# Optimization experiments

Hardware: AMD Instinct MI355X
Metric: run time of the kernel (lower is better)

The kernel has to match this reference:

```python
import jax, jax.numpy as jnp
import numpy as np

N_NODES = 20000
N_EDGES = 320000
N_GRAPHS = 16
NEG_SLOPE = 0.2


def gat_layer(x, src, dst, W, al, ar, b):
    # x: [N, F_in]; W: [F_in, H*D]; al/ar: [H, D]; b: [H*D]
    H, D = al.shape
    N = x.shape[0]
    f = (x @ W).reshape(N, H, D)                      # projected features [N,H,D]
    el = jnp.sum(f * al[None], axis=-1)                # [N,H]
    er = jnp.sum(f * ar[None], axis=-1)                # [N,H]
    e = jax.nn.leaky_relu(el[src] + er[dst], NEG_SLOPE)  # [E,H]
    # numerically stable segment softmax over incoming edges of each dst node
    m = jax.ops.segment_max(e, dst, num_segments=N)    # [N,H]
    m = jnp.where(jnp.isfinite(m), m, 0.0)
    ex = jnp.exp(e - m[dst])                           # [E,H]
    denom = jax.ops.segment_sum(ex, dst, num_segments=N)  # [N,H]
    msg = ex[:, :, None] * f[src]                      # [E,H,D]
    num = jax.ops.segment_sum(msg, dst, num_segments=N)   # [N,H,D]
    rst = num / jnp.where(denom > 0, denom, 1.0)[:, :, None]
    return rst + b.reshape(1, H, D)


def setup_inputs() -> dict:
    key = jax.random.key(0)
    ks = jax.random.split(key, 16)
    in_dim, hid, H = 128, 128, 3
    x = jax.random.normal(ks[0], (N_NODES, in_dim), dtype=jnp.float32)
    src = jax.random.randint(ks[1], (N_EDGES,), 0, N_NODES, dtype=jnp.int32)
    dst = jax.random.randint(ks[2], (N_EDGES,), 0, N_NODES, dtype=jnp.int32)
    graph_ids = jnp.sort(jax.random.randint(ks[3], (N_NODES,), 0, N_GRAPHS, dtype=jnp.int32))
    s = lambda d: 1.0 / np.sqrt(d)
    W1 = jax.random.normal(ks[4], (in_dim, H * hid), jnp.float32) * s(in_dim)
    al1 = jax.random.normal(ks[5], (H, hid), jnp.float32) * s(hid)
    ar1 = jax.random.normal(ks[6], (H, hid), jnp.float32) * s(hid)
    b1 = jnp.zeros((H * hid,), jnp.float32)
    W2 = jax.random.normal(ks[7], (H * hid, hid), jnp.float32) * s(H * hid)
    al2 = jax.random.normal(ks[8], (1, hid), jnp.float32) * s(hid)
    ar2 = jax.random.normal(ks[9], (1, hid), jnp.float32) * s(hid)
    b2 = jnp.zeros((hid,), jnp.float32)
    linW = jax.random.normal(ks[10], (hid, hid), jnp.float32) * s(hid)
    linb = jnp.zeros((hid,), jnp.float32)
    return dict(x=x, src=src, dst=dst, graph_ids=graph_ids, W1=W1, al1=al1,
                ar1=ar1, b1=b1, W2=W2, al2=al2, ar2=ar2, b2=b2, linW=linW, linb=linb)


def reference(x, src, dst, graph_ids, W1, al1, ar1, b1, W2, al2, ar2, b2, linW, linb):
    h = gat_layer(x, src, dst, W1, al1, ar1, b1)       # [N,3,hid]
    h = jax.nn.elu(h.reshape(h.shape[0], -1))          # [N,3*hid]
    h = gat_layer(h, src, dst, W2, al2, ar2, b2)       # [N,1,hid]
    h = h.squeeze(1)                                   # [N,hid]
    # dgl.mean_nodes over batched graph
    sums = jax.ops.segment_sum(h, graph_ids, num_segments=N_GRAPHS)      # [G,hid]
    cnts = jax.ops.segment_sum(jnp.ones_like(graph_ids, jnp.float32), graph_ids, num_segments=N_GRAPHS)
    hg = sums / jnp.maximum(cnts, 1.0)[:, None]
    return jax.nn.relu(hg @ linW + linb)
```

## Files before the change

### kernel.cpp

```cpp
#include <hip/hip_runtime.h>
#include <hip/hip_bf16.h>

#define NN 20000
#define NE 320000
#define NG 16
#define PSPLIT 32
#define NSCANB 79


__global__ void hist_kernel(const int* __restrict__ dst, int* __restrict__ indeg, int E) {
  int e = blockIdx.x * 256 + threadIdx.x;
  if (e < E) atomicAdd(&indeg[dst[e]], 1);
}

__global__ void scan1_kernel(const int* __restrict__ in, int* __restrict__ outp,
                             int* __restrict__ bsum, int n) {
  int b = blockIdx.x, t = threadIdx.x;
  int i = b * 256 + t;
  int lane = t & 63, wv = t >> 6;
  __shared__ int ws[4];
  int v = (i < n) ? in[i] : 0;
  int x = v;
#pragma unroll
  for (int off = 1; off < 64; off <<= 1) {
    int y = __shfl_up(x, off);
    if (lane >= off) x += y;
  }
  if (lane == 63) ws[wv] = x;
  __syncthreads();
  int add = 0;
  for (int w2 = 0; w2 < wv; w2++) add += ws[w2];
  x += add;
  if (i < n) outp[i] = x - v;
  if (t == 255) bsum[b] = x;
}

__global__ void scan2_kernel(const int* __restrict__ bsum, int* __restrict__ boff,
                             int* __restrict__ rp_end, int nb) {
  int t = threadIdx.x;
  int lane = t & 63, wv = t >> 6;
  __shared__ int ws[2];
  int v = (t < nb) ? bsum[t] : 0;
  int x = v;
#pragma unroll
  for (int off = 1; off < 64; off <<= 1) {
    int y = __shfl_up(x, off);
    if (lane >= off) x += y;
  }
  if (lane == 63) ws[wv] = x;
  __syncthreads();
  if (wv == 1) x += ws[0];
  if (t < nb) boff[t] = x - v;
  if (t == 127) *rp_end = x;
}

__global__ void scan3_kernel(int* __restrict__ outp, const int* __restrict__ boff, int n) {
  int i = blockIdx.x * 256 + threadIdx.x;
  if (i < n) outp[i] += boff[blockIdx.x];
}

__global__ void scatter_kernel(const int* __restrict__ src, const int* __restrict__ dst,
                               const int* __restrict__ rowptr, int* __restrict__ cursor,
                               int* __restrict__ csr_src, int E) {
  int e = blockIdx.x * 256 + threadIdx.x;
  if (e < E) {
    int d = dst[e];
    int p = atomicAdd(&cursor[d], 1);
    csr_src[rowptr[d] + p] = src[e];
  }
}


__global__ void prep_wlr_kernel(const float* __restrict__ W1, const float* __restrict__ al1,
                                const float* __restrict__ ar1, float* __restrict__ wlr) {
  int t = blockIdx.x * 256 + threadIdx.x;
  if (t >= 768) return;
  int k = t & 127;
  int j = t >> 7;
  int h = j % 3;
  const float* av = (j < 3 ? al1 : ar1) + h * 128;
  const float* wrow = W1 + (size_t)k * 384 + h * 128;
  float s = 0.f;
#pragma unroll 4
  for (int d = 0; d < 128; d++) s += wrow[d] * av[d];
  wlr[j * 128 + k] = s;
}

__global__ void elr_kernel(const float* __restrict__ x, const float* __restrict__ wlr,
                           float* __restrict__ el, float* __restrict__ er, int N) {
  __shared__ float wl_s[768];
  int t = threadIdx.x;
  for (int i = t; i < 768; i += 256) wl_s[i] = wlr[i];
  __syncthreads();
  int w = (blockIdx.x * 256 + t) >> 6;
  int lane = t & 63;
  if (w >= N) return;
  float v0 = x[(size_t)w * 128 + lane], v1 = x[(size_t)w * 128 + 64 + lane];
  float s[6];
#pragma unroll
  for (int j = 0; j < 6; j++) s[j] = v0 * wl_s[j * 128 + lane] + v1 * wl_s[j * 128 + 64 + lane];
#pragma unroll
  for (int off = 32; off; off >>= 1)
#pragma unroll
    for (int j = 0; j < 6; j++) s[j] += __shfl_down(s[j], off);
  if (lane == 0) {
    el[w * 3 + 0] = s[0]; el[w * 3 + 1] = s[1]; el[w * 3 + 2] = s[2];
    er[w * 3 + 0] = s[3]; er[w * 3 + 1] = s[4]; er[w * 3 + 2] = s[5];
  }
}


__global__ void aggregate_x_kernel(const float* __restrict__ x, const float* __restrict__ el,
                                   const float* __restrict__ er, const int* __restrict__ rowptr,
                                   const int* __restrict__ csr_src, float* __restrict__ aggx) {
  int n = blockIdx.x;
  int t = threadIdx.x;
  __shared__ float wbuf[3][128];
  __shared__ int sbuf[128];
  __shared__ float red[6];
  __shared__ float4 accbuf[3][4][32];
  int rs = rowptr[n];
  int deg = rowptr[n + 1] - rs;
  float er0 = er[n * 3 + 0], er1 = er[n * 3 + 1], er2 = er[n * 3 + 2];
  float p0 = 0.f, p1 = 0.f, p2 = 0.f;
  int g = t >> 5, dq = t & 31;
  const float* xd = x + dq * 4;
  float4 a0 = make_float4(0, 0, 0, 0), a1 = a0, a2 = a0;
  for (int base = 0; base < deg; base += 128) {
    int cnt = min(128, deg - base);
    if (t < cnt) {
      int s = csr_src[rs + base + t];
      sbuf[t] = s;
      float e0 = el[s * 3 + 0] + er0, e1 = el[s * 3 + 1] + er1, e2 = el[s * 3 + 2] + er2;
      e0 = e0 > 0.f ? e0 : 0.2f * e0;
      e1 = e1 > 0.f ? e1 : 0.2f * e1;
      e2 = e2 > 0.f ? e2 : 0.2f * e2;
      float w0 = __expf(e0), w1 = __expf(e1), w2 = __expf(e2);
      wbuf[0][t] = w0; wbuf[1][t] = w1; wbuf[2][t] = w2;
      p0 += w0; p1 += w1; p2 += w2;
    }
    __syncthreads();
    int j = g;
    for (; j + 4 < cnt; j += 8) {
      int s0 = sbuf[j], s1 = sbuf[j + 4];
      float4 v0 = *(const float4*)(xd + (size_t)s0 * 128);
      float4 v1 = *(const float4*)(xd + (size_t)s1 * 128);
      float w00 = wbuf[0][j], w01 = wbuf[1][j], w02 = wbuf[2][j];
      float w10 = wbuf[0][j + 4], w11 = wbuf[1][j + 4], w12 = wbuf[2][j + 4];
      a0.x += w00 * v0.x + w10 * v1.x; a0.y += w00 * v0.y + w10 * v1.y;
      a0.z += w00 * v0.z + w10 * v1.z; a0.w += w00 * v0.w + w10 * v1.w;
      a1.x += w01 * v0.x + w11 * v1.x; a1.y += w01 * v0.y + w11 * v1.y;
      a1.z += w01 * v0.z + w11 * v1.z; a1.w += w01 * v0.w + w11 * v1.w;
      a2.x += w02 * v0.x + w12 * v1.x; a2.y += w02 * v0.y + w12 * v1.y;
      a2.z += w02 * v0.z + w12 * v1.z; a2.w += w02 * v0.w + w12 * v1.w;
    }
    for (; j < cnt; j += 4) {
      int s = sbuf[j];
      float4 v = *(const float4*)(xd + (size_t)s * 128);
      float w0 = wbuf[0][j], w1 = wbuf[1][j], w2 = wbuf[2][j];
      a0.x += w0 * v.x; a0.y += w0 * v.y; a0.z += w0 * v.z; a0.w += w0 * v.w;
      a1.x += w1 * v.x; a1.y += w1 * v.y; a1.z += w1 * v.z; a1.w += w1 * v.w;
      a2.x += w2 * v.x; a2.y += w2 * v.y; a2.z += w2 * v.z; a2.w += w2 * v.w;
    }
    __syncthreads();
  }
  for (int off = 32; off; off >>= 1) {
    p0 += __shfl_down(p0, off);
    p1 += __shfl_down(p1, off);
    p2 += __shfl_down(p2, off);
  }
  int wv = t >> 6, ln = t & 63;
  if (ln == 0) { red[wv * 3 + 0] = p0; red[wv * 3 + 1] = p1; red[wv * 3 + 2] = p2; }
  accbuf[0][g][dq] = a0;
  accbuf[1][g][dq] = a1;
  accbuf[2][g][dq] = a2;
  __syncthreads();
  if (t < 96) {
    int h = t >> 5, d = t & 31;
    float4 s0 = accbuf[h][0][d], s1 = accbuf[h][1][d], s2 = accbuf[h][2][d], s3 = accbuf[h][3][d];
    float dn = red[h] + red[3 + h];
    float inv = dn > 0.f ? 1.f / dn : 0.f;
    float4 r;
    r.x = (s0.x + s1.x + s2.x + s3.x) * inv;
    r.y = (s0.y + s1.y + s2.y + s3.y) * inv;
    r.z = (s0.z + s1.z + s2.z + s3.z) * inv;
    r.w = (s0.w + s1.w + s2.w + s3.w) * inv;
    *(float4*)&aggx[(size_t)n * 384 + h * 128 + d * 4] = r;
  }
}


template <int NCB, bool SPLIT, bool BIAS_ELU>
__launch_bounds__(256, 2)
__global__ void gemm_8x8_kernel(const float* __restrict__ A, int lda,
                                const float* __restrict__ B, int ldb,
                                float* __restrict__ C, int ldc,
                                const float* __restrict__ bias) {
  __shared__ float4 As4[128 * 9];
  __shared__ float4 Bs4[32 * 33];
  int t = threadIdx.x;
  int tm = t >> 4, tn = t & 15;

  constexpr int NROWT = 157;
  constexpr int NWG = NROWT * NCB;
  constexpr int QW = NWG >> 3, RW = NWG & 7;
  int o = blockIdx.x;
  int xcd = o & 7, i8 = o >> 3;
  int wgid = (xcd < RW ? xcd * (QW + 1) : RW * (QW + 1) + (xcd - RW) * QW) + i8;
  int rt = wgid / NCB, cb = wgid - rt * NCB;
  int m0 = rt * 128;

  const float* Ab = A + (size_t)(cb * 128);
  const float* Bb = SPLIT ? B + (size_t)(cb * 128) * ldb : B + cb * 128;
  float* Cb = SPLIT ? C + (size_t)cb * NN * ldc : C + cb * 128;

  const float* sA[4];
  int dA[4];
#pragma unroll
  for (int p = 0; p < 4; ++p) {
    int r = p * 32 + (t >> 3);
    int row = m0 + r;
    if (row >= NN) row = NN - 1;
    sA[p] = Ab + (size_t)row * lda + (t & 7) * 4;
    dA[p] = r * 9 + (t & 7);
  }
  const float* sB[4];
  int dB[4];
#pragma unroll
  for (int p = 0; p < 4; ++p) {
    int kk = p * 8 + (t >> 5);
    sB[p] = Bb + (size_t)kk * ldb + (t & 31) * 4;
    dB[p] = kk * 33 + (t & 31);
  }

  float acc[8][8];
#pragma unroll
  for (int i = 0; i < 8; ++i)
#pragma unroll
    for (int c = 0; c < 8; ++c) acc[i][c] = 0.f;

  float4 pa[4], pb[4];
#pragma unroll
  for (int p = 0; p < 4; ++p) {
    pa[p] = *(const float4*)sA[p];
    pb[p] = *(const float4*)sB[p];
  }

  constexpr int NT = 4;
  for (int tk = 0; tk < NT; ++tk) {
#pragma unroll
    for (int p = 0; p < 4; ++p) {
      As4[dA[p]] = pa[p];
      Bs4[dB[p]] = pb[p];
    }
    __syncthreads();
    if (tk + 1 < NT) {
      int ko = (tk + 1) * 32;
#pragma unroll
      for (int p = 0; p < 4; ++p) {
        pa[p] = *(const float4*)(sA[p] + ko);
        pb[p] = *(const float4*)(sB[p] + (size_t)ko * ldb);
      }
    }
#pragma unroll
    for (int q = 0; q < 8; ++q) {
      float4 fa[8];
#pragma unroll
      for (int i = 0; i < 8; ++i) fa[i] = As4[(tm + 16 * i) * 9 + q];
#pragma unroll
      for (int j = 0; j < 4; ++j) {
        float4 b0 = Bs4[(4 * q + j) * 33 + tn];
        float4 b1 = Bs4[(4 * q + j) * 33 + 16 + tn];
#pragma unroll
        for (int i = 0; i < 8; ++i) {
          float a = (j == 0) ? fa[i].x : (j == 1) ? fa[i].y : (j == 2) ? fa[i].z : fa[i].w;
          acc[i][0] += a * b0.x; acc[i][1] += a * b0.y;
          acc[i][2] += a * b0.z; acc[i][3] += a * b0.w;
          acc[i][4] += a * b1.x; acc[i][5] += a * b1.y;
          acc[i][6] += a * b1.z; acc[i][7] += a * b1.w;
        }
      }
    }
    __syncthreads();
  }

  const float* bp0 = bias ? bias + cb * 128 + tn * 4 : nullptr;
#pragma unroll
  for (int i = 0; i < 8; ++i) {
    int row = m0 + tm + 16 * i;
    if (row < NN) {
      float* Cr = Cb + (size_t)row * ldc + tn * 4;
      float4 v0 = make_float4(acc[i][0], acc[i][1], acc[i][2], acc[i][3]);
      float4 v1 = make_float4(acc[i][4], acc[i][5], acc[i][6], acc[i][7]);
      if (BIAS_ELU) {
        v0.x += bp0[0]; v0.y += bp0[1]; v0.z += bp0[2]; v0.w += bp0[3];
        v1.x += bp0[64]; v1.y += bp0[65]; v1.z += bp0[66]; v1.w += bp0[67];
        v0.x = v0.x > 0.f ? v0.x : expm1f(v0.x);
        v0.y = v0.y > 0.f ? v0.y : expm1f(v0.y);
        v0.z = v0.z > 0.f ? v0.z : expm1f(v0.z);
        v0.w = v0.w > 0.f ? v0.w : expm1f(v0.w);
        v1.x = v1.x > 0.f ? v1.x : expm1f(v1.x);
        v1.y = v1.y > 0.f ? v1.y : expm1f(v1.y);
        v1.z = v1.z > 0.f ? v1.z : expm1f(v1.z);
        v1.w = v1.w > 0.f ? v1.w : expm1f(v1.w);
      }
      *(float4*)Cr = v0;
      *(float4*)(Cr + 64) = v1;
    }
  }
}


__global__ void att_combine_kernel(const float* __restrict__ fp, const float* __restrict__ al,
                                   const float* __restrict__ ar, float* __restrict__ f2,
                                   float* __restrict__ el, float* __restrict__ er, int N) {
  int w = (blockIdx.x * 256 + threadIdx.x) >> 6;
  int lane = threadIdx.x & 63;
  if (w >= N) return;
  size_t base = (size_t)w * 128;
  const size_t PS = (size_t)NN * 128;
  float v0 = fp[base + lane] + fp[PS + base + lane] + fp[2 * PS + base + lane];
  float v1 = fp[base + 64 + lane] + fp[PS + base + 64 + lane] + fp[2 * PS + base + 64 + lane];
  f2[base + lane] = v0;
  f2[base + 64 + lane] = v1;
  float se = v0 * al[lane] + v1 * al[64 + lane];
  float sr = v0 * ar[lane] + v1 * ar[64 + lane];
  for (int off = 32; off; off >>= 1) {
    se += __shfl_down(se, off);
    sr += __shfl_down(sr, off);
  }
  if (lane == 0) { el[w] = se; er[w] = sr; }
}


__global__ void aggregate1_kernel(const float* __restrict__ f, const float* __restrict__ el,
                                  const float* __restrict__ er, const float* __restrict__ bias,
                                  const int* __restrict__ rowptr, const int* __restrict__ csr_src,
                                  float* __restrict__ out) {
  int n = blockIdx.x;
  int t = threadIdx.x;
  __shared__ float wbuf[128];
  __shared__ int sbuf[128];
  __shared__ float red[2];
  __shared__ float4 accbuf[4][32];
  int rs = rowptr[n];
  int deg = rowptr[n + 1] - rs;
  float ern = er[n];
  float psum = 0.f;
  int g = t >> 5;
  int d = (t & 31) * 4;
  const float* fd = f + d;
  float4 acc = make_float4(0.f, 0.f, 0.f, 0.f);
  for (int base = 0; base < deg; base += 128) {
    int cnt = min(128, deg - base);
    if (t < cnt) {
      int s = csr_src[rs + base + t];
      sbuf[t] = s;
      float e = el[s] + ern;
      e = e > 0.f ? e : 0.2f * e;
      float w = __expf(e);
      wbuf[t] = w;
      psum += w;
    }
    __syncthreads();
    int j = g;
    for (; j + 4 < cnt; j += 8) {
      int s0 = sbuf[j], s1 = sbuf[j + 4];
      float4 v0 = *(const float4*)(fd + (size_t)s0 * 128);
      float4 v1 = *(const float4*)(fd + (size_t)s1 * 128);
      float w0 = wbuf[j], w1 = wbuf[j + 4];
      acc.x += w0 * v0.x + w1 * v1.x;
      acc.y += w0 * v0.y + w1 * v1.y;
      acc.z += w0 * v0.z + w1 * v1.z;
      acc.w += w0 * v0.w + w1 * v1.w;
    }
    for (; j < cnt; j += 4) {
      int s = sbuf[j];
      float4 v = *(const float4*)(fd + (size_t)s * 128);
      float w = wbuf[j];
      acc.x += w * v.x; acc.y += w * v.y; acc.z += w * v.z; acc.w += w * v.w;
    }
    __syncthreads();
  }
  for (int off = 32; off; off >>= 1) psum += __shfl_down(psum, off);
  int wv = t >> 6, ln = t & 63;
  if (ln == 0) red[wv] = psum;
  accbuf[g][t & 31] = acc;
  __syncthreads();
  if (t < 32) {
    float4 a0 = accbuf[0][t], a1 = accbuf[1][t], a2 = accbuf[2][t], a3 = accbuf[3][t];
    float dn = red[0] + red[1];
    float inv = dn > 0.f ? 1.f / dn : 0.f;
    const float* bp = bias + t * 4;
    float4 r;
    r.x = (a0.x + a1.x + a2.x + a3.x) * inv + bp[0];
    r.y = (a0.y + a1.y + a2.y + a3.y) * inv + bp[1];
    r.z = (a0.z + a1.z + a2.z + a3.z) * inv + bp[2];
    r.w = (a0.w + a1.w + a2.w + a3.w) * inv + bp[3];
    *(float4*)&out[(size_t)n * 128 + t * 4] = r;
  }
}


__global__ void pool_partial_kernel(const float* __restrict__ h2, const int* __restrict__ gid,
                                    float* __restrict__ sums, int N) {
  int g = blockIdx.x / PSPLIT;
  int sp = blockIdx.x % PSPLIT;
  int tid = threadIdx.x;
  int lo0 = 0, hi0 = N;
  while (lo0 < hi0) { int m = (lo0 + hi0) >> 1; if (gid[m] < g) lo0 = m + 1; else hi0 = m; }
  int lo1 = lo0, hi1 = N;
  while (lo1 < hi1) { int m = (lo1 + hi1) >> 1; if (gid[m] < g + 1) lo1 = m + 1; else hi1 = m; }
  float a0 = 0.f, a1 = 0.f, a2 = 0.f, a3 = 0.f;
  int n = lo0 + sp;
  for (; n + 3 * PSPLIT < lo1; n += 4 * PSPLIT) {
    a0 += h2[(size_t)n * 128 + tid];
    a1 += h2[(size_t)(n + PSPLIT) * 128 + tid];
    a2 += h2[(size_t)(n + 2 * PSPLIT) * 128 + tid];
    a3 += h2[(size_t)(n + 3 * PSPLIT) * 128 + tid];
  }
  for (; n < lo1; n += PSPLIT) a0 += h2[(size_t)n * 128 + tid];
  float acc = (a0 + a1) + (a2 + a3);
  atomicAdd(&sums[g * 128 + tid], acc);
}

__global__ void pool_final_kernel(const float* __restrict__ sums, const int* __restrict__ gid,
                                  const float* __restrict__ linW, const float* __restrict__ linb,
                                  float* __restrict__ out, int N) {
  int g = blockIdx.x;
  int tid = threadIdx.x;
  int lo0 = 0, hi0 = N;
  while (lo0 < hi0) { int m = (lo0 + hi0) >> 1; if (gid[m] < g) lo0 = m + 1; else hi0 = m; }
  int lo1 = lo0, hi1 = N;
  while (lo1 < hi1) { int m = (lo1 + hi1) >> 1; if (gid[m] < g + 1) lo1 = m + 1; else hi1 = m; }
  int cnt = lo1 - lo0;
  float hg = sums[g * 128 + tid] / (float)(cnt > 0 ? cnt : 1);
  __shared__ float hgs[128];
  hgs[tid] = hg;
  __syncthreads();
  float o = linb[tid];
#pragma unroll 4
  for (int dd = 0; dd < 128; dd++) o += hgs[dd] * linW[dd * 128 + tid];
  out[g * 128 + tid] = fmaxf(o, 0.f);
}


extern "C" void kernel_launch(void* const* d_in, const int* in_sizes, int n_in,
                              void* d_out, int out_size, void* d_ws, size_t ws_size,
                              hipStream_t stream) {
  const float* x    = (const float*)d_in[0];
  const int*   src  = (const int*)d_in[1];
  const int*   dst  = (const int*)d_in[2];
  const int*   gid  = (const int*)d_in[3];
  const float* W1   = (const float*)d_in[4];
  const float* al1  = (const float*)d_in[5];
  const float* ar1  = (const float*)d_in[6];
  const float* b1   = (const float*)d_in[7];
  const float* W2   = (const float*)d_in[8];
  const float* al2  = (const float*)d_in[9];
  const float* ar2  = (const float*)d_in[10];
  const float* b2   = (const float*)d_in[11];
  const float* linW = (const float*)d_in[12];
  const float* linb = (const float*)d_in[13];
  float* out = (float*)d_out;

  char* ws = (char*)d_ws;
  size_t off = 0;
  auto alloc = [&](size_t bytes) -> void* {
    void* p = ws + off;
    off += (bytes + 255) & ~(size_t)255;
    return p;
  };
  float* aggx    = (float*)alloc((size_t)NN * 384 * 4);
  float* h1      = (float*)alloc((size_t)NN * 384 * 4);
  float* f2      = (float*)alloc((size_t)NN * 128 * 4);
  float* h2      = (float*)alloc((size_t)NN * 128 * 4);
  float* el1     = (float*)alloc((size_t)NN * 3 * 4);
  float* er1     = (float*)alloc((size_t)NN * 3 * 4);
  float* el2     = (float*)alloc((size_t)NN * 4);
  float* er2     = (float*)alloc((size_t)NN * 4);
  float* wlr     = (float*)alloc((size_t)768 * 4);
  int*   rowptr  = (int*)alloc((size_t)(NN + 1) * 4);
  int*   csr_src = (int*)alloc((size_t)NE * 4);
  int*   bsum    = (int*)alloc((size_t)NSCANB * 4);
  int*   boff    = (int*)alloc((size_t)NSCANB * 4);
  int*   indeg   = (int*)alloc((size_t)NN * 4);
  int*   cursor  = (int*)alloc((size_t)NN * 4);
  float* gsums   = (float*)alloc((size_t)NG * 128 * 4);
  (void)ws_size;
  size_t zbytes = (char*)(gsums + NG * 128) - (char*)indeg;
  hipMemsetAsync(indeg, 0, zbytes, stream);

  hist_kernel<<<(NE + 255) / 256, 256, 0, stream>>>(dst, indeg, NE);
  scan1_kernel<<<NSCANB, 256, 0, stream>>>(indeg, rowptr, bsum, NN);
  scan2_kernel<<<1, 128, 0, stream>>>(bsum, boff, rowptr + NN, NSCANB);
  scan3_kernel<<<NSCANB, 256, 0, stream>>>(rowptr, boff, NN);
  scatter_kernel<<<(NE + 255) / 256, 256, 0, stream>>>(src, dst, rowptr, cursor, csr_src, NE);

  prep_wlr_kernel<<<3, 256, 0, stream>>>(W1, al1, ar1, wlr);
  elr_kernel<<<(NN + 3) / 4, 256, 0, stream>>>(x, wlr, el1, er1, NN);
  aggregate_x_kernel<<<NN, 128, 0, stream>>>(x, el1, er1, rowptr, csr_src, aggx);
  gemm_8x8_kernel<3, false, true><<<157 * 3, 256, 0, stream>>>(
      aggx, 384, W1, 384, h1, 384, b1);

  float* fpart = aggx;
  gemm_8x8_kernel<3, true, false><<<157 * 3, 256, 0, stream>>>(
      h1, 384, W2, 128, fpart, 128, nullptr);
  att_combine_kernel<<<(NN + 3) / 4, 256, 0, stream>>>(fpart, al2, ar2, f2, el2, er2, NN);
  aggregate1_kernel<<<NN, 128, 0, stream>>>(f2, el2, er2, b2, rowptr, csr_src, h2);

  pool_partial_kernel<<<NG * PSPLIT, 128, 0, stream>>>(h2, gid, gsums, NN);
  pool_final_kernel<<<NG, 128, 0, stream>>>(gsums, gid, linW, linb, out, NN);
}
```

Before: 306.4 us.

## Double-buffer GEMM shared tiles with k=16 steps and XOR swizzle

The FP32 GEMM kernel now uses two shared-memory buffers with a K-step of 16 instead of one buffer with a K-step of 32. The next tile is written to the alternate buffer while the current one is consumed, which removes one barrier per iteration. Padding of the A tile is replaced by an XOR swizzle to avoid bank conflicts. There are more iterations (8 instead of 4), and shared memory usage stays roughly the same.

```diff
diff --git a/kernel.cpp b/kernel.cpp
--- a/kernel.cpp
+++ b/kernel.cpp
@@ -192,12 +192,12 @@
 
 template <int NCB, bool SPLIT, bool BIAS_ELU>
 __launch_bounds__(256, 2)
-__global__ void gemm_8x8_kernel(const float* __restrict__ A, int lda,
-                                const float* __restrict__ B, int ldb,
-                                float* __restrict__ C, int ldc,
-                                const float* __restrict__ bias) {
-  __shared__ float4 As4[128 * 9];
-  __shared__ float4 Bs4[32 * 33];
+__global__ void gemm_dbuf_kernel(const float* __restrict__ A, int lda,
+                                 const float* __restrict__ B, int ldb,
+                                 float* __restrict__ C, int ldc,
+                                 const float* __restrict__ bias) {
+  __shared__ float4 Asb[2][128 * 4];
+  __shared__ float4 Bsb[2][16 * 32];
   int t = threadIdx.x;
   int tm = t >> 4, tn = t & 15;
 
@@ -214,23 +214,25 @@
   const float* Bb = SPLIT ? B + (size_t)(cb * 128) * ldb : B + cb * 128;
   float* Cb = SPLIT ? C + (size_t)cb * NN * ldc : C + cb * 128;
 
-  const float* sA[4];
-  int dA[4];
-#pragma unroll
-  for (int p = 0; p < 4; ++p) {
-    int r = p * 32 + (t >> 3);
+  const float* sA[2];
+  int dA[2];
+#pragma unroll
+  for (int p = 0; p < 2; ++p) {
+    int idx = p * 256 + t;
+    int r = idx >> 2, qh = idx & 3;
     int row = m0 + r;
     if (row >= NN) row = NN - 1;
-    sA[p] = Ab + (size_t)row * lda + (t & 7) * 4;
-    dA[p] = r * 9 + (t & 7);
-  }
-  const float* sB[4];
-  int dB[4];
-#pragma unroll
-  for (int p = 0; p < 4; ++p) {
-    int kk = p * 8 + (t >> 5);
-    sB[p] = Bb + (size_t)kk * ldb + (t & 31) * 4;
-    dB[p] = kk * 33 + (t & 31);
+    sA[p] = Ab + (size_t)row * lda + qh * 4;
+    dA[p] = r * 4 + (qh ^ (r & 3));
+  }
+  const float* sB[2];
+  int dB[2];
+#pragma unroll
+  for (int p = 0; p < 2; ++p) {
+    int idx = p * 256 + t;
+    int kk = idx >> 5, n4 = idx & 31;
+    sB[p] = Bb + (size_t)kk * ldb + n4 * 4;
+    dB[p] = kk * 32 + n4;
   }
 
   float acc[8][8];
@@ -239,38 +241,31 @@
 #pragma unroll
     for (int c = 0; c < 8; ++c) acc[i][c] = 0.f;
 
-  float4 pa[4], pb[4];
-#pragma unroll
-  for (int p = 0; p < 4; ++p) {
-    pa[p] = *(const float4*)sA[p];
-    pb[p] = *(const float4*)sB[p];
-  }
-
-  constexpr int NT = 4;
-  for (int tk = 0; tk < NT; ++tk) {
-#pragma unroll
-    for (int p = 0; p < 4; ++p) {
-      As4[dA[p]] = pa[p];
-      Bs4[dB[p]] = pb[p];
-    }
-    __syncthreads();
-    if (tk + 1 < NT) {
-      int ko = (tk + 1) * 32;
-#pragma unroll
-      for (int p = 0; p < 4; ++p) {
-        pa[p] = *(const float4*)(sA[p] + ko);
-        pb[p] = *(const float4*)(sB[p] + (size_t)ko * ldb);
-      }
-    }
-#pragma unroll
-    for (int q = 0; q < 8; ++q) {
+  float4 pa[2], pb[2];
+#pragma unroll
+  for (int p = 0; p < 2; ++p) { pa[p] = *(const float4*)sA[p]; pb[p] = *(const float4*)sB[p]; }
+#pragma unroll
+  for (int p = 0; p < 2; ++p) { Asb[0][dA[p]] = pa[p]; Bsb[0][dB[p]] = pb[p]; }
+  __syncthreads();
+#pragma unroll
+  for (int p = 0; p < 2; ++p) {
+    pa[p] = *(const float4*)(sA[p] + 16);
+    pb[p] = *(const float4*)(sB[p] + (size_t)16 * ldb);
+  }
+
+  for (int h = 0; h < 8; ++h) {
+    int c = h & 1;
+#pragma unroll
+    for (int qh = 0; qh < 4; ++qh) {
       float4 fa[8];
 #pragma unroll
-      for (int i = 0; i < 8; ++i) fa[i] = As4[(tm + 16 * i) * 9 + q];
+      for (int i = 0; i < 8; ++i)
+        fa[i] = Asb[c][(tm + 16 * i) * 4 + (qh ^ (tm & 3))];
 #pragma unroll
       for (int j = 0; j < 4; ++j) {
-        float4 b0 = Bs4[(4 * q + j) * 33 + tn];
-        float4 b1 = Bs4[(4 * q + j) * 33 + 16 + tn];
+        int kk = qh * 4 + j;
+        float4 b0 = Bsb[c][kk * 32 + tn];
+        float4 b1 = Bsb[c][kk * 32 + 16 + tn];
 #pragma unroll
         for (int i = 0; i < 8; ++i) {
           float a = (j == 0) ? fa[i].x : (j == 1) ? fa[i].y : (j == 2) ? fa[i].z : fa[i].w;
@@ -279,6 +274,18 @@
           acc[i][4] += a * b1.x; acc[i][5] += a * b1.y;
           acc[i][6] += a * b1.z; acc[i][7] += a * b1.w;
         }
+      }
+    }
+    if (h + 1 < 8) {
+#pragma unroll
+      for (int p = 0; p < 2; ++p) { Asb[c ^ 1][dA[p]] = pa[p]; Bsb[c ^ 1][dB[p]] = pb[p]; }
+    }
+    if (h + 2 < 8) {
+      int ko = (h + 2) * 16;
+#pragma unroll
+      for (int p = 0; p < 2; ++p) {
+        pa[p] = *(const float4*)(sA[p] + ko);
+        pb[p] = *(const float4*)(sB[p] + (size_t)ko * ldb);
       }
     }
     __syncthreads();
@@ -500,11 +507,11 @@
   prep_wlr_kernel<<<3, 256, 0, stream>>>(W1, al1, ar1, wlr);
   elr_kernel<<<(NN + 3) / 4, 256, 0, stream>>>(x, wlr, el1, er1, NN);
   aggregate_x_kernel<<<NN, 128, 0, stream>>>(x, el1, er1, rowptr, csr_src, aggx);
-  gemm_8x8_kernel<3, false, true><<<157 * 3, 256, 0, stream>>>(
+  gemm_dbuf_kernel<3, false, true><<<157 * 3, 256, 0, stream>>>(
       aggx, 384, W1, 384, h1, 384, b1);
 
   float* fpart = aggx;
-  gemm_8x8_kernel<3, true, false><<<157 * 3, 256, 0, stream>>>(
+  gemm_dbuf_kernel<3, true, false><<<157 * 3, 256, 0, stream>>>(
       h1, 384, W2, 128, fpart, 128, nullptr);
   att_combine_kernel<<<(NN + 3) / 4, 256, 0, stream>>>(fpart, al2, ar2, f2, el2, er2, NN);
   aggregate1_kernel<<<NN, 128, 0, stream>>>(f2, el2, er2, b2, rowptr, csr_src, h2);
```

Result: slower. 523.4 us (+70.8%).

## Rewrite GEMM to read wave-uniform B via scalar loads, halve column tile

Applied to the files above, without the earlier changes.

The tiled GEMM no longer stages B in LDS. Each wave takes a wave-uniform 16-column slice of B (readfirstlane), so the compiler can fetch it with scalar loads, while each lane computes two rows by 16 columns from the A tile in shared memory. The column tile drops from 128 to 64, which doubles the workgroup count, and launch bounds rise to 4 waves per SIMD. This removes B's LDS traffic and most A LDS reads per FMA. The cost is many scalar memory loads per k step and lower arithmetic reuse per thread, since A is now read twice as often overall.

```diff
diff --git a/kernel.cpp b/kernel.cpp
--- a/kernel.cpp
+++ b/kernel.cpp
@@ -191,15 +191,15 @@
 
 
 template <int NCB, bool SPLIT, bool BIAS_ELU>
-__launch_bounds__(256, 2)
-__global__ void gemm_8x8_kernel(const float* __restrict__ A, int lda,
-                                const float* __restrict__ B, int ldb,
-                                float* __restrict__ C, int ldc,
-                                const float* __restrict__ bias) {
+__launch_bounds__(256, 4)
+__global__ void gemm_sgprB_kernel(const float* __restrict__ A, int lda,
+                                  const float* __restrict__ B, int ldb,
+                                  float* __restrict__ C, int ldc,
+                                  const float* __restrict__ bias) {
   __shared__ float4 As4[128 * 9];
-  __shared__ float4 Bs4[32 * 33];
   int t = threadIdx.x;
-  int tm = t >> 4, tn = t & 15;
+  int lane = t & 63;
+  int w = t >> 6;
 
   constexpr int NROWT = 157;
   constexpr int NWG = NROWT * NCB;
@@ -210,104 +210,88 @@
   int rt = wgid / NCB, cb = wgid - rt * NCB;
   int m0 = rt * 128;
 
-  const float* Ab = A + (size_t)(cb * 128);
-  const float* Bb = SPLIT ? B + (size_t)(cb * 128) * ldb : B + cb * 128;
-  float* Cb = SPLIT ? C + (size_t)cb * NN * ldc : C + cb * 128;
+  const float* Ab = A + (size_t)((cb >> 1) * 128);
+  const float* Bb = SPLIT ? B + (size_t)((cb >> 1) * 128) * ldb + (cb & 1) * 64
+                          : B + cb * 64;
+  float* Cb = SPLIT ? C + (size_t)(cb >> 1) * NN * ldc + (cb & 1) * 64
+                    : C + cb * 64;
+
+  int wu = __builtin_amdgcn_readfirstlane(w);
+  const float* Bw = Bb + wu * 16;
 
   const float* sA[4];
   int dA[4];
 #pragma unroll
   for (int p = 0; p < 4; ++p) {
-    int r = p * 32 + (t >> 3);
+    int idx = p * 256 + t;
+    int r = idx >> 3, q = idx & 7;
     int row = m0 + r;
     if (row >= NN) row = NN - 1;
-    sA[p] = Ab + (size_t)row * lda + (t & 7) * 4;
-    dA[p] = r * 9 + (t & 7);
-  }
-  const float* sB[4];
-  int dB[4];
-#pragma unroll
-  for (int p = 0; p < 4; ++p) {
-    int kk = p * 8 + (t >> 5);
-    sB[p] = Bb + (size_t)kk * ldb + (t & 31) * 4;
-    dB[p] = kk * 33 + (t & 31);
-  }
-
-  float acc[8][8];
-#pragma unroll
-  for (int i = 0; i < 8; ++i)
-#pragma unroll
-    for (int c = 0; c < 8; ++c) acc[i][c] = 0.f;
-
-  float4 pa[4], pb[4];
-#pragma unroll
-  for (int p = 0; p < 4; ++p) {
-    pa[p] = *(const float4*)sA[p];
-    pb[p] = *(const float4*)sB[p];
-  }
-
-  constexpr int NT = 4;
-  for (int tk = 0; tk < NT; ++tk) {
-#pragma unroll
-    for (int p = 0; p < 4; ++p) {
-      As4[dA[p]] = pa[p];
-      Bs4[dB[p]] = pb[p];
-    }
-    __syncthreads();
-    if (tk + 1 < NT) {
-      int ko = (tk + 1) * 32;
-#pragma unroll
-      for (int p = 0; p < 4; ++p) {
-        pa[p] = *(const float4*)(sA[p] + ko);
-        pb[p] = *(const float4*)(sB[p] + (size_t)ko * ldb);
-      }
+    sA[p] = Ab + (size_t)row * lda + q * 4;
+    dA[p] = r * 9 + q;
+  }
+
+  float acc0[16], acc1[16];
+#pragma unroll
+  for (int c = 0; c < 16; ++c) { acc0[c] = 0.f; acc1[c] = 0.f; }
+
+  float4 pa[4];
+#pragma unroll
+  for (int p = 0; p < 4; ++p) pa[p] = *(const float4*)sA[p];
+
+  for (int k0 = 0; k0 < 128; k0 += 32) {
+#pragma unroll
+    for (int p = 0; p < 4; ++p) As4[dA[p]] = pa[p];
+    __syncthreads();
+    if (k0 + 32 < 128) {
+#pragma unroll
+      for (int p = 0; p < 4; ++p) pa[p] = *(const float4*)(sA[p] + k0 + 32);
     }
 #pragma unroll
     for (int q = 0; q < 8; ++q) {
-      float4 fa[8];
-#pragma unroll
-      for (int i = 0; i < 8; ++i) fa[i] = As4[(tm + 16 * i) * 9 + q];
+      float4 fa0 = As4[lane * 9 + q];
+      float4 fa1 = As4[(lane + 64) * 9 + q];
+      float a0f[4] = {fa0.x, fa0.y, fa0.z, fa0.w};
+      float a1f[4] = {fa1.x, fa1.y, fa1.z, fa1.w};
 #pragma unroll
       for (int j = 0; j < 4; ++j) {
-        float4 b0 = Bs4[(4 * q + j) * 33 + tn];
-        float4 b1 = Bs4[(4 * q + j) * 33 + 16 + tn];
-#pragma unroll
-        for (int i = 0; i < 8; ++i) {
-          float a = (j == 0) ? fa[i].x : (j == 1) ? fa[i].y : (j == 2) ? fa[i].z : fa[i].w;
-          acc[i][0] += a * b0.x; acc[i][1] += a * b0.y;
-          acc[i][2] += a * b0.z; acc[i][3] += a * b0.w;
-          acc[i][4] += a * b1.x; acc[i][5] += a * b1.y;
-          acc[i][6] += a * b1.z; acc[i][7] += a * b1.w;
+        const float* Bk = Bw + (size_t)(k0 + q * 4 + j) * ldb;
+        float a0 = a0f[j], a1 = a1f[j];
+#pragma unroll
+        for (int c = 0; c < 16; ++c) {
+          float bv = Bk[c];
+          acc0[c] += a0 * bv;
+          acc1[c] += a1 * bv;
         }
       }
     }
     __syncthreads();
   }
 
-  const float* bp0 = bias ? bias + cb * 128 + tn * 4 : nullptr;
-#pragma unroll
-  for (int i = 0; i < 8; ++i) {
-    int row = m0 + tm + 16 * i;
+  int colv = (SPLIT ? (cb & 1) * 64 : cb * 64) + w * 16;
+#pragma unroll
+  for (int rr = 0; rr < 2; ++rr) {
+    int row = m0 + lane + rr * 64;
     if (row < NN) {
-      float* Cr = Cb + (size_t)row * ldc + tn * 4;
-      float4 v0 = make_float4(acc[i][0], acc[i][1], acc[i][2], acc[i][3]);
-      float4 v1 = make_float4(acc[i][4], acc[i][5], acc[i][6], acc[i][7]);
-      if (BIAS_ELU) {
-        v0.x += bp0[0]; v0.y += bp0[1]; v0.z += bp0[2]; v0.w += bp0[3];
-        v1.x += bp0[64]; v1.y += bp0[65]; v1.z += bp0[66]; v1.w += bp0[67];
-        v0.x = v0.x > 0.f ? v0.x : expm1f(v0.x);
-        v0.y = v0.y > 0.f ? v0.y : expm1f(v0.y);
-        v0.z = v0.z > 0.f ? v0.z : expm1f(v0.z);
-        v0.w = v0.w > 0.f ? v0.w : expm1f(v0.w);
-        v1.x = v1.x > 0.f ? v1.x : expm1f(v1.x);
-        v1.y = v1.y > 0.f ? v1.y : expm1f(v1.y);
-        v1.z = v1.z > 0.f ? v1.z : expm1f(v1.z);
-        v1.w = v1.w > 0.f ? v1.w : expm1f(v1.w);
+      float* Cr = Cb + (size_t)row * ldc + w * 16;
+      const float* av = rr ? acc1 : acc0;
+#pragma unroll
+      for (int cc = 0; cc < 4; ++cc) {
+        float4 v = make_float4(av[cc * 4 + 0], av[cc * 4 + 1],
+                               av[cc * 4 + 2], av[cc * 4 + 3]);
+        if (BIAS_ELU) {
+          const float* bp = bias + cb * 64 + w * 16 + cc * 4;
+          v.x += bp[0]; v.y += bp[1]; v.z += bp[2]; v.w += bp[3];
+          v.x = v.x > 0.f ? v.x : expm1f(v.x);
+          v.y = v.y > 0.f ? v.y : expm1f(v.y);
+          v.z = v.z > 0.f ? v.z : expm1f(v.z);
+          v.w = v.w > 0.f ? v.w : expm1f(v.w);
+        }
+        *(float4*)(Cr + cc * 4) = v;
       }
-      *(float4*)Cr = v0;
-      *(float4*)(Cr + 64) = v1;
-    }
-  }
+    }
+  }
+  (void)colv;
 }
 
 
@@ -500,11 +484,11 @@
   prep_wlr_kernel<<<3, 256, 0, stream>>>(W1, al1, ar1, wlr);
   elr_kernel<<<(NN + 3) / 4, 256, 0, stream>>>(x, wlr, el1, er1, NN);
   aggregate_x_kernel<<<NN, 128, 0, stream>>>(x, el1, er1, rowptr, csr_src, aggx);
-  gemm_8x8_kernel<3, false, true><<<157 * 3, 256, 0, stream>>>(
+  gemm_sgprB_kernel<6, false, true><<<157 * 6, 256, 0, stream>>>(
       aggx, 384, W1, 384, h1, 384, b1);
 
   float* fpart = aggx;
-  gemm_8x8_kernel<3, true, false><<<157 * 3, 256, 0, stream>>>(
+  gemm_sgprB_kernel<6, true, false><<<157 * 6, 256, 0, stream>>>(
       h1, 384, W2, 128, fpart, 128, nullptr);
   att_combine_kernel<<<(NN + 3) / 4, 256, 0, stream>>>(fpart, al2, ar2, f2, el2, er2, NN);
   aggregate1_kernel<<<NN, 128, 0, stream>>>(f2, el2, er2, b2, rowptr, csr_src, h2);
```

New measurement: 313.0 us. +2.1%, slower.
